# Kernel tuning notes

Measured on AMD Instinct MI355X. Metric: run time of the kernel, lower is better.

## Reference

```python
import jax, jax.numpy as jnp
import numpy as np

H = 128          # hidden size
D = 2048         # input size
B, T = 64, 256   # batch, seq_len


def _lstm_layer(x_proj, Whh, h0, c0):
    """x_proj: [B,T,4H] precomputed input projection (+ both biases).
    Returns (full hidden sequence [B,T,H], final hidden [B,H]).
    PyTorch gate order: i, f, g, o."""
    def step(carry, xt):
        h, c = carry
        g = xt + h @ Whh.T                      # [B,4H]
        i, f, gg, o = jnp.split(g, 4, axis=-1)
        i = jax.nn.sigmoid(i)
        f = jax.nn.sigmoid(f)
        gg = jnp.tanh(gg)
        o = jax.nn.sigmoid(o)
        c = f * c + i * gg
        h = o * jnp.tanh(c)
        return (h, c), h

    (hT, _), hs = jax.lax.scan(step, (h0, c0), jnp.swapaxes(x_proj, 0, 1))
    return jnp.swapaxes(hs, 0, 1), hT


def setup_inputs() -> dict:
    key = jax.random.key(0)
    ks = jax.random.split(key, 11)
    k = 1.0 / np.sqrt(H)  # torch default init bound
    u = lambda kk, shape: jax.random.uniform(kk, shape, jnp.float32, -k, k)
    return {
        "x":    jax.random.normal(ks[0], (B, T, D), jnp.float32),
        "Wih0": u(ks[1], (4 * H, D)),
        "Whh0": u(ks[2], (4 * H, H)),
        "bih0": u(ks[3], (4 * H,)),
        "bhh0": u(ks[4], (4 * H,)),
        "Wih1": u(ks[5], (4 * H, H)),
        "Whh1": u(ks[6], (4 * H, H)),
        "bih1": u(ks[7], (4 * H,)),
        "bhh1": u(ks[8], (4 * H,)),
        "Wfc":  u(ks[9], (1, H)),
        "bfc":  u(ks[10], (1,)),
    }


def reference(x, Wih0, Whh0, bih0, bhh0, Wih1, Whh1, bih1, bhh1, Wfc, bfc):
    b = x.shape[0]
    h0 = jnp.zeros((b, H), x.dtype)
    # layer 0: batch the big input GEMM across all timesteps
    xp0 = jnp.einsum('btd,gd->btg', x, Wih0) + bih0 + bhh0   # [B,T,4H]
    seq0, _ = _lstm_layer(xp0, Whh0, h0, h0)
    # layer 1 (dropout disabled in eval)
    xp1 = jnp.einsum('bth,gh->btg', seq0, Wih1) + bih1 + bhh1
    _, hT = _lstm_layer(xp1, Whh1, h0, h0)                   # h_n[-1]
    return hT @ Wfc.T + bfc                                  # [B,1]
```

## Files before the change

### kernel.cpp

```cpp
#include <hip/hip_runtime.h>
#include <math.h>

#define HH 128
#define DD 2048
#define BATCH 64
#define TT 256
#define G4 512
#define GB 16
#define HPAD 136

typedef __attribute__((ext_vector_type(8))) short bf16x8;
typedef __attribute__((ext_vector_type(4))) float f32x4;
typedef _Float16 f16x8 __attribute__((ext_vector_type(8)));


static __device__ __forceinline__ unsigned short f2bf_rne(float f) {
    union { float f; unsigned u; } v; v.f = f;
    unsigned r = v.u + 0x7fff + ((v.u >> 16) & 1);
    return (unsigned short)(r >> 16);
}
static __device__ __forceinline__ float bf2f(unsigned short b) {
    union { unsigned u; float f; } v; v.u = ((unsigned)b) << 16;
    return v.f;
}
static __device__ __forceinline__ float fexp2(float x) {
#if __has_builtin(__builtin_amdgcn_exp2f)
    return __builtin_amdgcn_exp2f(x);
#else
    return exp2f(x);
#endif
}
static __device__ __forceinline__ float frcp(float x) {
#if __has_builtin(__builtin_amdgcn_rcpf)
    return __builtin_amdgcn_rcpf(x);
#else
    return 1.f / x;
#endif
}
static __device__ __forceinline__ float sigmoid_f(float x) {
    return frcp(1.f + fexp2(-1.44269504f * x));
}
static __device__ __forceinline__ float tanh_f(float x) {
    float xx = fminf(fmaxf(x, -15.f), 15.f);
    float e = fexp2(2.88539008f * xx);
    return 1.f - 2.f * frcp(e + 1.f);
}

#define PK 40

__global__ __launch_bounds__(256) void gemm_split_bf16(
    const float* __restrict__ A, const float* __restrict__ Bw,
    const float* __restrict__ b1, const float* __restrict__ b2,
    float* __restrict__ C, int M, int N, int K)
{
    __shared__ unsigned short Ah[128 * PK], Al[128 * PK];
    __shared__ unsigned short Bh[128 * PK], Bl[128 * PK];

    const int tid = threadIdx.x;
    const int l = tid & 63;
    const int w = tid >> 6;
    const int wr = w >> 1, wc = w & 1;
    const int bm = blockIdx.y, bn = blockIdx.x;

    f32x4 acc[4][4];
#pragma unroll
    for (int m = 0; m < 4; ++m)
#pragma unroll
        for (int n = 0; n < 4; ++n) acc[m][n] = f32x4{0.f, 0.f, 0.f, 0.f};

    const float* Ab = A + (size_t)(bm * 128) * K;

    for (int k0 = 0; k0 < K; k0 += 32) {
        __syncthreads();
#pragma unroll
        for (int q = 0; q < 4; ++q) {
            int fid = tid + 256 * q;
            int r = fid >> 3;
            int kk = (fid & 7) << 2;
            int n = bn * 128 + r;
            int orign = ((n & 3) << 7) | (n >> 2);
            float4 av = *(const float4*)(Ab + (size_t)r * K + k0 + kk);
            float4 bv = *(const float4*)(Bw + (size_t)orign * K + k0 + kk);
            float a4[4] = {av.x, av.y, av.z, av.w};
            float b4[4] = {bv.x, bv.y, bv.z, bv.w};
            ushort4 ahv, alv, bhv, blv;
            unsigned short t;
            t = f2bf_rne(a4[0]); ahv.x = t; alv.x = f2bf_rne(a4[0] - bf2f(t));
            t = f2bf_rne(a4[1]); ahv.y = t; alv.y = f2bf_rne(a4[1] - bf2f(t));
            t = f2bf_rne(a4[2]); ahv.z = t; alv.z = f2bf_rne(a4[2] - bf2f(t));
            t = f2bf_rne(a4[3]); ahv.w = t; alv.w = f2bf_rne(a4[3] - bf2f(t));
            t = f2bf_rne(b4[0]); bhv.x = t; blv.x = f2bf_rne(b4[0] - bf2f(t));
            t = f2bf_rne(b4[1]); bhv.y = t; blv.y = f2bf_rne(b4[1] - bf2f(t));
            t = f2bf_rne(b4[2]); bhv.z = t; blv.z = f2bf_rne(b4[2] - bf2f(t));
            t = f2bf_rne(b4[3]); bhv.w = t; blv.w = f2bf_rne(b4[3] - bf2f(t));
            int off = r * PK + kk;
            *(ushort4*)&Ah[off] = ahv;
            *(ushort4*)&Al[off] = alv;
            *(ushort4*)&Bh[off] = bhv;
            *(ushort4*)&Bl[off] = blv;
        }
        __syncthreads();

        bf16x8 aH[4], aL[4], bH[4], bL[4];
#pragma unroll
        for (int m = 0; m < 4; ++m) {
            int row = wr * 64 + m * 16 + (l & 15);
            int off = row * PK + 8 * (l >> 4);
            aH[m] = *(const bf16x8*)&Ah[off];
            aL[m] = *(const bf16x8*)&Al[off];
        }
#pragma unroll
        for (int n = 0; n < 4; ++n) {
            int row = wc * 64 + n * 16 + (l & 15);
            int off = row * PK + 8 * (l >> 4);
            bH[n] = *(const bf16x8*)&Bh[off];
            bL[n] = *(const bf16x8*)&Bl[off];
        }
#pragma unroll
        for (int m = 0; m < 4; ++m)
#pragma unroll
            for (int n = 0; n < 4; ++n) {
                acc[m][n] = __builtin_amdgcn_mfma_f32_16x16x32_bf16(aH[m], bH[n], acc[m][n], 0, 0, 0);
                acc[m][n] = __builtin_amdgcn_mfma_f32_16x16x32_bf16(aH[m], bL[n], acc[m][n], 0, 0, 0);
                acc[m][n] = __builtin_amdgcn_mfma_f32_16x16x32_bf16(aL[m], bH[n], acc[m][n], 0, 0, 0);
            }
    }

#pragma unroll
    for (int n = 0; n < 4; ++n) {
        int cg = bn * 128 + wc * 64 + n * 16 + (l & 15);
        int orig = ((cg & 3) << 7) | (cg >> 2);
        float bias = b1[orig] + b2[orig];
        size_t cbase = (size_t)(cg >> 6) * 1024 + ((cg >> 4) & 3) * 256 + (cg & 15);
#pragma unroll
        for (int m = 0; m < 4; ++m) {
            int r0 = bm * 128 + wr * 64 + m * 16 + ((l >> 4) << 2);
            f32x4 v = acc[m][n];
#pragma unroll
            for (int i = 0; i < 4; ++i) {
                int r = r0 + i;
                int t = r & 255, b = r >> 8;
                C[(size_t)t * 32768 + (size_t)(b >> 4) * 8192 + cbase + (b & 15) * 16] = v[i] + bias;
            }
        }
    }
}

__global__ void prep_bias1(const float* __restrict__ bih1,
                           const float* __restrict__ bhh1,
                           float* __restrict__ bias1p)
{
    int n = threadIdx.x;
    int orig = ((n & 3) << 7) | (n >> 2);
    bias1p[n] = bih1[orig] + bhh1[orig];
}

__global__ __launch_bounds__(512) void lstm_fused(
    const float* __restrict__ xp,
    const float* __restrict__ Whh0,
    const float* __restrict__ Wih1,
    const float* __restrict__ Whh1,
    const float* __restrict__ bias1p,
    const float* __restrict__ Wfc,
    const float* __restrict__ bfc,
    float* __restrict__ out)
{
    const int tid = threadIdx.x;
    const int l  = tid & 63;
    const int w  = tid >> 6;
    const int lb = l & 15;
    const int lg = l >> 4;
    const int blk = blockIdx.x;

    __shared__ ushort h0b[2][GB][HPAD];
    __shared__ ushort h1b[2][GB][HPAD];
    __shared__ float red[8][GB];

    for (int i = tid; i < 2 * GB * HPAD; i += 512) {
        ((ushort*)h0b)[i] = 0;
        ((ushort*)h1b)[i] = 0;
    }

    f16x8 wf0[4][4], wi1[4][4], wh1[4][4];
#pragma unroll
    for (int mm = 0; mm < 4; ++mm) {
        int rp = (w * 4 + mm) * 16 + lb;
        int orig = ((rp & 3) << 7) | (rp >> 2);
#pragma unroll
        for (int kt = 0; kt < 4; ++kt) {
            const float* p0 = Whh0 + (size_t)orig * HH + kt * 32 + lg * 8;
            const float* p1 = Wih1 + (size_t)orig * HH + kt * 32 + lg * 8;
            const float* p2 = Whh1 + (size_t)orig * HH + kt * 32 + lg * 8;
            float4 a0 = *(const float4*)p0, a1 = *(const float4*)(p0 + 4);
            float4 b0 = *(const float4*)p1, b1v = *(const float4*)(p1 + 4);
            float4 c0v = *(const float4*)p2, c1v = *(const float4*)(p2 + 4);
            f16x8 f;
            f[0]=(_Float16)a0.x; f[1]=(_Float16)a0.y; f[2]=(_Float16)a0.z; f[3]=(_Float16)a0.w;
            f[4]=(_Float16)a1.x; f[5]=(_Float16)a1.y; f[6]=(_Float16)a1.z; f[7]=(_Float16)a1.w;
            wf0[mm][kt] = f;
            f[0]=(_Float16)b0.x; f[1]=(_Float16)b0.y; f[2]=(_Float16)b0.z; f[3]=(_Float16)b0.w;
            f[4]=(_Float16)b1v.x; f[5]=(_Float16)b1v.y; f[6]=(_Float16)b1v.z; f[7]=(_Float16)b1v.w;
            wi1[mm][kt] = f;
            f[0]=(_Float16)c0v.x; f[1]=(_Float16)c0v.y; f[2]=(_Float16)c0v.z; f[3]=(_Float16)c0v.w;
            f[4]=(_Float16)c1v.x; f[5]=(_Float16)c1v.y; f[6]=(_Float16)c1v.z; f[7]=(_Float16)c1v.w;
            wh1[mm][kt] = f;
        }
    }

    const float* xbase = xp + (size_t)blk * 8192 + w * 1024 + lb * 16 + lg * 4;
    const int ubase = w * 16 + lg;

    f32x4 X[4];
#pragma unroll
    for (int mm = 0; mm < 4; ++mm) X[mm] = *(const f32x4*)(xbase + mm * 256);

    float c0[4] = {0.f,0.f,0.f,0.f}, c1[4] = {0.f,0.f,0.f,0.f}, hv[4];
    __syncthreads();

#pragma unroll
    for (int mm = 0; mm < 4; ++mm) {
        float iv = sigmoid_f(X[mm][0]);
        float fv = sigmoid_f(X[mm][1]);
        float gg = tanh_f(X[mm][2]);
        float ov = sigmoid_f(X[mm][3]);
        float c = fmaf(fv, 0.f, iv * gg);
        c0[mm] = c;
        float h = ov * tanh_f(c);
        union { _Float16 f; ushort s; } hc; hc.f = (_Float16)h;
        h0b[0][lb][ubase + mm * 4] = hc.s;
    }
#pragma unroll
    for (int mm = 0; mm < 4; ++mm)
        X[mm] = *(const f32x4*)(xbase + 32768 + mm * 256);
    __syncthreads();

    for (int p = 0; p < TT; ++p) {
        const int rb = p & 1, wb = rb ^ 1;

        f32x4 a0[4], a1[4];
#pragma unroll
        for (int mm = 0; mm < 4; ++mm) a0[mm] = X[mm];
#pragma unroll
        for (int mm = 0; mm < 4; ++mm)
            a1[mm] = *(const f32x4*)(bias1p + (w * 4 + mm) * 16 + lg * 4);

#pragma unroll
        for (int kt = 0; kt < 4; ++kt) {
            union { uint4 u; f16x8 h; } cvt;
            cvt.u = *(const uint4*)&h0b[rb][lb][kt * 32 + lg * 8];
            f16x8 bh = cvt.h;
#pragma unroll
            for (int mm = 0; mm < 4; ++mm)
                a0[mm] = __builtin_amdgcn_mfma_f32_16x16x32_f16(wf0[mm][kt], bh, a0[mm], 0, 0, 0);
#pragma unroll
            for (int mm = 0; mm < 4; ++mm)
                a1[mm] = __builtin_amdgcn_mfma_f32_16x16x32_f16(wi1[mm][kt], bh, a1[mm], 0, 0, 0);
        }
#pragma unroll
        for (int kt = 0; kt < 4; ++kt) {
            union { uint4 u; f16x8 h; } cvt;
            cvt.u = *(const uint4*)&h1b[rb][lb][kt * 32 + lg * 8];
            f16x8 bh = cvt.h;
#pragma unroll
            for (int mm = 0; mm < 4; ++mm)
                a1[mm] = __builtin_amdgcn_mfma_f32_16x16x32_f16(wh1[mm][kt], bh, a1[mm], 0, 0, 0);
        }

        int tn = (p + 2 < TT) ? p + 2 : TT - 1;
#pragma unroll
        for (int mm = 0; mm < 4; ++mm)
            X[mm] = *(const f32x4*)(xbase + (size_t)tn * 32768 + mm * 256);

#pragma unroll
        for (int mm = 0; mm < 4; ++mm) {
            float iv = sigmoid_f(a0[mm][0]);
            float fv = sigmoid_f(a0[mm][1]);
            float gg = tanh_f(a0[mm][2]);
            float ov = sigmoid_f(a0[mm][3]);
            float c = fmaf(fv, c0[mm], iv * gg);
            c0[mm] = c;
            float h = ov * tanh_f(c);
            union { _Float16 f; ushort s; } hc; hc.f = (_Float16)h;
            h0b[wb][lb][ubase + mm * 4] = hc.s;
        }
#pragma unroll
        for (int mm = 0; mm < 4; ++mm) {
            float iv = sigmoid_f(a1[mm][0]);
            float fv = sigmoid_f(a1[mm][1]);
            float gg = tanh_f(a1[mm][2]);
            float ov = sigmoid_f(a1[mm][3]);
            float c = fmaf(fv, c1[mm], iv * gg);
            c1[mm] = c;
            float h = ov * tanh_f(c);
            hv[mm] = h;
            union { _Float16 f; ushort s; } hc; hc.f = (_Float16)h;
            h1b[wb][lb][ubase + mm * 4] = hc.s;
        }
        __syncthreads();
    }

    float pr = 0.f;
#pragma unroll
    for (int mm = 0; mm < 4; ++mm)
        pr = fmaf(hv[mm], Wfc[ubase + mm * 4], pr);
    pr += __shfl_xor(pr, 16, 64);
    pr += __shfl_xor(pr, 32, 64);
    if (l < GB) red[w][l] = pr;
    __syncthreads();
    if (tid < GB) {
        float s = bfc[0];
#pragma unroll
        for (int q = 0; q < 8; ++q) s += red[q][tid];
        out[blk * GB + tid] = s;
    }
}

extern "C" void kernel_launch(void* const* d_in, const int* in_sizes, int n_in,
                              void* d_out, int out_size, void* d_ws, size_t ws_size,
                              hipStream_t stream)
{
    const float* x    = (const float*)d_in[0];
    const float* Wih0 = (const float*)d_in[1];
    const float* Whh0 = (const float*)d_in[2];
    const float* bih0 = (const float*)d_in[3];
    const float* bhh0 = (const float*)d_in[4];
    const float* Wih1 = (const float*)d_in[5];
    const float* Whh1 = (const float*)d_in[6];
    const float* bih1 = (const float*)d_in[7];
    const float* bhh1 = (const float*)d_in[8];
    const float* Wfc  = (const float*)d_in[9];
    const float* bfc  = (const float*)d_in[10];
    float* out = (float*)d_out;

    const int M = BATCH * TT;
    float* xp      = (float*)d_ws;
    float* bias1p  = xp + (size_t)M * G4;

    gemm_split_bf16<<<dim3(G4 / 128, M / 128), 256, 0, stream>>>(
        x, Wih0, bih0, bhh0, xp, M, G4, DD);

    prep_bias1<<<1, G4, 0, stream>>>(bih1, bhh1, bias1p);

    lstm_fused<<<BATCH / GB, 512, 0, stream>>>(
        xp, Whh0, Wih1, Whh1, bias1p, Wfc, bfc, out);
}
```

Measured before the change: 902.0 us.

## Split LSTM recurrence over 16 waves and use packed bf16 conversion in GEMM

The fused LSTM kernel now runs 1024 threads (16 waves) per block, so each wave owns 2 gate tiles instead of 4. This halves the serial MFMA and activation work per wave on every timestep. To fit registers, the layer-1 recurrent weights are moved from registers to LDS and reloaded each step. Layer-0 activations are computed before the layer-1 recurrent MFMAs. Separately, the split-bf16 input GEMM replaces the software rounding with the hardware packed v_cvt_pk_bf16_f32 instruction. This adds LDS traffic and more waves joining each barrier in exchange for a shorter per-step critical path.

```diff
diff --git a/kernel.cpp b/kernel.cpp
--- a/kernel.cpp
+++ b/kernel.cpp
@@ -14,14 +14,10 @@
 typedef _Float16 f16x8 __attribute__((ext_vector_type(8)));
 
 
-static __device__ __forceinline__ unsigned short f2bf_rne(float f) {
-    union { float f; unsigned u; } v; v.f = f;
-    unsigned r = v.u + 0x7fff + ((v.u >> 16) & 1);
-    return (unsigned short)(r >> 16);
-}
-static __device__ __forceinline__ float bf2f(unsigned short b) {
-    union { unsigned u; float f; } v; v.u = ((unsigned)b) << 16;
-    return v.f;
+static __device__ __forceinline__ unsigned cvt_pk_bf16(float a, float b) {
+    unsigned r;
+    asm("v_cvt_pk_bf16_f32 %0, %1, %2" : "=v"(r) : "v"(a), "v"(b));
+    return r;
 }
 static __device__ __forceinline__ float fexp2(float x) {
 #if __has_builtin(__builtin_amdgcn_exp2f)
@@ -44,6 +40,17 @@
     float xx = fminf(fmaxf(x, -15.f), 15.f);
     float e = fexp2(2.88539008f * xx);
     return 1.f - 2.f * frcp(e + 1.f);
+}
+static __device__ __forceinline__ ushort hbits(float h) {
+    union { _Float16 f; ushort s; } u; u.f = (_Float16)h; return u.s;
+}
+static __device__ __forceinline__ float lstm_cell(const f32x4 g, float& c) {
+    float iv = sigmoid_f(g[0]);
+    float fv = sigmoid_f(g[1]);
+    float gg = tanh_f(g[2]);
+    float ov = sigmoid_f(g[3]);
+    c = fmaf(fv, c, iv * gg);
+    return ov * tanh_f(c);
 }
 
 #define PK 40
@@ -81,23 +88,23 @@
             int orign = ((n & 3) << 7) | (n >> 2);
             float4 av = *(const float4*)(Ab + (size_t)r * K + k0 + kk);
             float4 bv = *(const float4*)(Bw + (size_t)orign * K + k0 + kk);
-            float a4[4] = {av.x, av.y, av.z, av.w};
-            float b4[4] = {bv.x, bv.y, bv.z, bv.w};
-            ushort4 ahv, alv, bhv, blv;
-            unsigned short t;
-            t = f2bf_rne(a4[0]); ahv.x = t; alv.x = f2bf_rne(a4[0] - bf2f(t));
-            t = f2bf_rne(a4[1]); ahv.y = t; alv.y = f2bf_rne(a4[1] - bf2f(t));
-            t = f2bf_rne(a4[2]); ahv.z = t; alv.z = f2bf_rne(a4[2] - bf2f(t));
-            t = f2bf_rne(a4[3]); ahv.w = t; alv.w = f2bf_rne(a4[3] - bf2f(t));
-            t = f2bf_rne(b4[0]); bhv.x = t; blv.x = f2bf_rne(b4[0] - bf2f(t));
-            t = f2bf_rne(b4[1]); bhv.y = t; blv.y = f2bf_rne(b4[1] - bf2f(t));
-            t = f2bf_rne(b4[2]); bhv.z = t; blv.z = f2bf_rne(b4[2] - bf2f(t));
-            t = f2bf_rne(b4[3]); bhv.w = t; blv.w = f2bf_rne(b4[3] - bf2f(t));
             int off = r * PK + kk;
-            *(ushort4*)&Ah[off] = ahv;
-            *(ushort4*)&Al[off] = alv;
-            *(ushort4*)&Bh[off] = bhv;
-            *(ushort4*)&Bl[off] = blv;
+            unsigned h01 = cvt_pk_bf16(av.x, av.y), h23 = cvt_pk_bf16(av.z, av.w);
+            float l0 = av.x - __uint_as_float(h01 << 16);
+            float l1 = av.y - __uint_as_float(h01 & 0xffff0000u);
+            float l2 = av.z - __uint_as_float(h23 << 16);
+            float l3 = av.w - __uint_as_float(h23 & 0xffff0000u);
+            unsigned lo01 = cvt_pk_bf16(l0, l1), lo23 = cvt_pk_bf16(l2, l3);
+            *(uint2*)&Ah[off] = uint2{h01, h23};
+            *(uint2*)&Al[off] = uint2{lo01, lo23};
+            h01 = cvt_pk_bf16(bv.x, bv.y); h23 = cvt_pk_bf16(bv.z, bv.w);
+            l0 = bv.x - __uint_as_float(h01 << 16);
+            l1 = bv.y - __uint_as_float(h01 & 0xffff0000u);
+            l2 = bv.z - __uint_as_float(h23 << 16);
+            l3 = bv.w - __uint_as_float(h23 & 0xffff0000u);
+            lo01 = cvt_pk_bf16(l0, l1); lo23 = cvt_pk_bf16(l2, l3);
+            *(uint2*)&Bh[off] = uint2{h01, h23};
+            *(uint2*)&Bl[off] = uint2{lo01, lo23};
         }
         __syncthreads();
 
@@ -155,7 +162,7 @@
     bias1p[n] = bih1[orig] + bhh1[orig];
 }
 
-__global__ __launch_bounds__(512) void lstm_fused(
+__global__ __launch_bounds__(1024) void lstm_fused16(
     const float* __restrict__ xp,
     const float* __restrict__ Whh0,
     const float* __restrict__ Wih1,
@@ -174,135 +181,112 @@
 
     __shared__ ushort h0b[2][GB][HPAD];
     __shared__ ushort h1b[2][GB][HPAD];
-    __shared__ float red[8][GB];
-
-    for (int i = tid; i < 2 * GB * HPAD; i += 512) {
+    __shared__ float red[16][GB];
+    __shared__ _Float16 W1[32 * 4 * 64 * 8];
+
+    for (int i = tid; i < 2 * GB * HPAD; i += 1024) {
         ((ushort*)h0b)[i] = 0;
         ((ushort*)h1b)[i] = 0;
     }
 
-    f16x8 wf0[4][4], wi1[4][4], wh1[4][4];
-#pragma unroll
-    for (int mm = 0; mm < 4; ++mm) {
-        int rp = (w * 4 + mm) * 16 + lb;
+    f16x8 wf0[2][4], wi1[2][4];
+#pragma unroll
+    for (int i = 0; i < 2; ++i) {
+        int mt = 2 * w + i;
+        int rp = mt * 16 + lb;
         int orig = ((rp & 3) << 7) | (rp >> 2);
+        const float* p0 = Whh0 + (size_t)orig * HH;
+        const float* p1 = Wih1 + (size_t)orig * HH;
+        const float* p2 = Whh1 + (size_t)orig * HH;
 #pragma unroll
         for (int kt = 0; kt < 4; ++kt) {
-            const float* p0 = Whh0 + (size_t)orig * HH + kt * 32 + lg * 8;
-            const float* p1 = Wih1 + (size_t)orig * HH + kt * 32 + lg * 8;
-            const float* p2 = Whh1 + (size_t)orig * HH + kt * 32 + lg * 8;
-            float4 a0 = *(const float4*)p0, a1 = *(const float4*)(p0 + 4);
-            float4 b0 = *(const float4*)p1, b1v = *(const float4*)(p1 + 4);
-            float4 c0v = *(const float4*)p2, c1v = *(const float4*)(p2 + 4);
+            float4 x0, x1;
             f16x8 f;
-            f[0]=(_Float16)a0.x; f[1]=(_Float16)a0.y; f[2]=(_Float16)a0.z; f[3]=(_Float16)a0.w;
-            f[4]=(_Float16)a1.x; f[5]=(_Float16)a1.y; f[6]=(_Float16)a1.z; f[7]=(_Float16)a1.w;
-            wf0[mm][kt] = f;
-            f[0]=(_Float16)b0.x; f[1]=(_Float16)b0.y; f[2]=(_Float16)b0.z; f[3]=(_Float16)b0.w;
-            f[4]=(_Float16)b1v.x; f[5]=(_Float16)b1v.y; f[6]=(_Float16)b1v.z; f[7]=(_Float16)b1v.w;
-            wi1[mm][kt] = f;
-            f[0]=(_Float16)c0v.x; f[1]=(_Float16)c0v.y; f[2]=(_Float16)c0v.z; f[3]=(_Float16)c0v.w;
-            f[4]=(_Float16)c1v.x; f[5]=(_Float16)c1v.y; f[6]=(_Float16)c1v.z; f[7]=(_Float16)c1v.w;
-            wh1[mm][kt] = f;
-        }
-    }
-
-    const float* xbase = xp + (size_t)blk * 8192 + w * 1024 + lb * 16 + lg * 4;
-    const int ubase = w * 16 + lg;
-
-    f32x4 X[4];
-#pragma unroll
-    for (int mm = 0; mm < 4; ++mm) X[mm] = *(const f32x4*)(xbase + mm * 256);
-
-    float c0[4] = {0.f,0.f,0.f,0.f}, c1[4] = {0.f,0.f,0.f,0.f}, hv[4];
+            x0 = *(const float4*)(p0 + kt * 32 + lg * 8);
+            x1 = *(const float4*)(p0 + kt * 32 + lg * 8 + 4);
+            f[0]=(_Float16)x0.x; f[1]=(_Float16)x0.y; f[2]=(_Float16)x0.z; f[3]=(_Float16)x0.w;
+            f[4]=(_Float16)x1.x; f[5]=(_Float16)x1.y; f[6]=(_Float16)x1.z; f[7]=(_Float16)x1.w;
+            wf0[i][kt] = f;
+            x0 = *(const float4*)(p1 + kt * 32 + lg * 8);
+            x1 = *(const float4*)(p1 + kt * 32 + lg * 8 + 4);
+            f[0]=(_Float16)x0.x; f[1]=(_Float16)x0.y; f[2]=(_Float16)x0.z; f[3]=(_Float16)x0.w;
+            f[4]=(_Float16)x1.x; f[5]=(_Float16)x1.y; f[6]=(_Float16)x1.z; f[7]=(_Float16)x1.w;
+            wi1[i][kt] = f;
+            x0 = *(const float4*)(p2 + kt * 32 + lg * 8);
+            x1 = *(const float4*)(p2 + kt * 32 + lg * 8 + 4);
+            f[0]=(_Float16)x0.x; f[1]=(_Float16)x0.y; f[2]=(_Float16)x0.z; f[3]=(_Float16)x0.w;
+            f[4]=(_Float16)x1.x; f[5]=(_Float16)x1.y; f[6]=(_Float16)x1.z; f[7]=(_Float16)x1.w;
+            *(f16x8*)&W1[((size_t)(mt * 4 + kt) * 64 + l) * 8] = f;
+        }
+    }
+
+    const float* xb = xp + (size_t)blk * 8192 + lb * 16 + lg * 4;
+    auto xaddr = [&](int t, int i) {
+        int mt = 2 * w + i;
+        return xb + (size_t)t * 32768 + (mt >> 2) * 1024 + (mt & 3) * 256;
+    };
+
+    f32x4 Xa = *(const f32x4*)xaddr(0, 0);
+    f32x4 Xb = *(const f32x4*)xaddr(0, 1);
+
+    float c0[2] = {0.f, 0.f}, c1[2] = {0.f, 0.f}, hv[2];
     __syncthreads();
 
-#pragma unroll
-    for (int mm = 0; mm < 4; ++mm) {
-        float iv = sigmoid_f(X[mm][0]);
-        float fv = sigmoid_f(X[mm][1]);
-        float gg = tanh_f(X[mm][2]);
-        float ov = sigmoid_f(X[mm][3]);
-        float c = fmaf(fv, 0.f, iv * gg);
-        c0[mm] = c;
-        float h = ov * tanh_f(c);
-        union { _Float16 f; ushort s; } hc; hc.f = (_Float16)h;
-        h0b[0][lb][ubase + mm * 4] = hc.s;
-    }
-#pragma unroll
-    for (int mm = 0; mm < 4; ++mm)
-        X[mm] = *(const f32x4*)(xbase + 32768 + mm * 256);
+    {
+        float h;
+        h = lstm_cell(Xa, c0[0]);  h0b[0][lb][8 * w + lg]     = hbits(h);
+        h = lstm_cell(Xb, c0[1]);  h0b[0][lb][8 * w + 4 + lg] = hbits(h);
+    }
+    Xa = *(const f32x4*)xaddr(1, 0);
+    Xb = *(const f32x4*)xaddr(1, 1);
     __syncthreads();
 
     for (int p = 0; p < TT; ++p) {
         const int rb = p & 1, wb = rb ^ 1;
 
-        f32x4 a0[4], a1[4];
-#pragma unroll
-        for (int mm = 0; mm < 4; ++mm) a0[mm] = X[mm];
-#pragma unroll
-        for (int mm = 0; mm < 4; ++mm)
-            a1[mm] = *(const f32x4*)(bias1p + (w * 4 + mm) * 16 + lg * 4);
+        f32x4 A00 = Xa, A01 = Xb;
+        {
+            int tn = (p + 2 < TT) ? p + 2 : TT - 1;
+            Xa = *(const f32x4*)xaddr(tn, 0);
+            Xb = *(const f32x4*)xaddr(tn, 1);
+        }
+        f32x4 A10 = *(const f32x4*)(bias1p + (2 * w) * 16 + lg * 4);
+        f32x4 A11 = *(const f32x4*)(bias1p + (2 * w + 1) * 16 + lg * 4);
 
 #pragma unroll
         for (int kt = 0; kt < 4; ++kt) {
             union { uint4 u; f16x8 h; } cvt;
             cvt.u = *(const uint4*)&h0b[rb][lb][kt * 32 + lg * 8];
             f16x8 bh = cvt.h;
-#pragma unroll
-            for (int mm = 0; mm < 4; ++mm)
-                a0[mm] = __builtin_amdgcn_mfma_f32_16x16x32_f16(wf0[mm][kt], bh, a0[mm], 0, 0, 0);
-#pragma unroll
-            for (int mm = 0; mm < 4; ++mm)
-                a1[mm] = __builtin_amdgcn_mfma_f32_16x16x32_f16(wi1[mm][kt], bh, a1[mm], 0, 0, 0);
+            A00 = __builtin_amdgcn_mfma_f32_16x16x32_f16(wf0[0][kt], bh, A00, 0, 0, 0);
+            A01 = __builtin_amdgcn_mfma_f32_16x16x32_f16(wf0[1][kt], bh, A01, 0, 0, 0);
+            A10 = __builtin_amdgcn_mfma_f32_16x16x32_f16(wi1[0][kt], bh, A10, 0, 0, 0);
+            A11 = __builtin_amdgcn_mfma_f32_16x16x32_f16(wi1[1][kt], bh, A11, 0, 0, 0);
+        }
+        {
+            float h;
+            h = lstm_cell(A00, c0[0]);  h0b[wb][lb][8 * w + lg]     = hbits(h);
+            h = lstm_cell(A01, c0[1]);  h0b[wb][lb][8 * w + 4 + lg] = hbits(h);
         }
 #pragma unroll
         for (int kt = 0; kt < 4; ++kt) {
             union { uint4 u; f16x8 h; } cvt;
             cvt.u = *(const uint4*)&h1b[rb][lb][kt * 32 + lg * 8];
             f16x8 bh = cvt.h;
-#pragma unroll
-            for (int mm = 0; mm < 4; ++mm)
-                a1[mm] = __builtin_amdgcn_mfma_f32_16x16x32_f16(wh1[mm][kt], bh, a1[mm], 0, 0, 0);
-        }
-
-        int tn = (p + 2 < TT) ? p + 2 : TT - 1;
-#pragma unroll
-        for (int mm = 0; mm < 4; ++mm)
-            X[mm] = *(const f32x4*)(xbase + (size_t)tn * 32768 + mm * 256);
-
-#pragma unroll
-        for (int mm = 0; mm < 4; ++mm) {
-            float iv = sigmoid_f(a0[mm][0]);
-            float fv = sigmoid_f(a0[mm][1]);
-            float gg = tanh_f(a0[mm][2]);
-            float ov = sigmoid_f(a0[mm][3]);
-            float c = fmaf(fv, c0[mm], iv * gg);
-            c0[mm] = c;
-            float h = ov * tanh_f(c);
-            union { _Float16 f; ushort s; } hc; hc.f = (_Float16)h;
-            h0b[wb][lb][ubase + mm * 4] = hc.s;
-        }
-#pragma unroll
-        for (int mm = 0; mm < 4; ++mm) {
-            float iv = sigmoid_f(a1[mm][0]);
-            float fv = sigmoid_f(a1[mm][1]);
-            float gg = tanh_f(a1[mm][2]);
-            float ov = sigmoid_f(a1[mm][3]);
-            float c = fmaf(fv, c1[mm], iv * gg);
-            c1[mm] = c;
-            float h = ov * tanh_f(c);
-            hv[mm] = h;
-            union { _Float16 f; ushort s; } hc; hc.f = (_Float16)h;
-            h1b[wb][lb][ubase + mm * 4] = hc.s;
+            f16x8 w0 = *(const f16x8*)&W1[((size_t)((2 * w) * 4 + kt) * 64 + l) * 8];
+            f16x8 w1 = *(const f16x8*)&W1[((size_t)((2 * w + 1) * 4 + kt) * 64 + l) * 8];
+            A10 = __builtin_amdgcn_mfma_f32_16x16x32_f16(w0, bh, A10, 0, 0, 0);
+            A11 = __builtin_amdgcn_mfma_f32_16x16x32_f16(w1, bh, A11, 0, 0, 0);
+        }
+        {
+            float h;
+            h = lstm_cell(A10, c1[0]);  hv[0] = h;  h1b[wb][lb][8 * w + lg]     = hbits(h);
+            h = lstm_cell(A11, c1[1]);  hv[1] = h;  h1b[wb][lb][8 * w + 4 + lg] = hbits(h);
         }
         __syncthreads();
     }
 
-    float pr = 0.f;
-#pragma unroll
-    for (int mm = 0; mm < 4; ++mm)
-        pr = fmaf(hv[mm], Wfc[ubase + mm * 4], pr);
+    float pr = fmaf(hv[0], Wfc[8 * w + lg], hv[1] * Wfc[8 * w + 4 + lg]);
     pr += __shfl_xor(pr, 16, 64);
     pr += __shfl_xor(pr, 32, 64);
     if (l < GB) red[w][l] = pr;
@@ -310,7 +294,7 @@
     if (tid < GB) {
         float s = bfc[0];
 #pragma unroll
-        for (int q = 0; q < 8; ++q) s += red[q][tid];
+        for (int q = 0; q < 16; ++q) s += red[q][tid];
         out[blk * GB + tid] = s;
     }
 }
@@ -341,6 +325,6 @@
 
     prep_bias1<<<1, G4, 0, stream>>>(bih1, bhh1, bias1p);
 
-    lstm_fused<<<BATCH / GB, 512, 0, stream>>>(
+    lstm_fused16<<<BATCH / GB, 1024, 0, stream>>>(
         xp, Whh0, Wih1, Whh1, bias1p, Wfc, bfc, out);
 }
```

Result: faster. 872.1 us (-3.3%).
